# Kernel tuning notes

Measured on AMD Instinct MI355X. Metric: run time of the kernel, lower is better.

## Reference

```python
import jax, jax.numpy as jnp
import numpy as np

N_NODES = 50000
N_EDGES = 800000
D_IN = 128
D_HID = 128
D_OUT = 128


def _gcn_layer(x, W, b, src, dst, norm):
    # dense projection then edge-weighted gather -> scatter-add at dst
    h = x @ W                                   # [N, d_out]
    msg = h[src] * norm[:, None]                # [E, d_out]
    out = jax.ops.segment_sum(msg, dst, num_segments=N_NODES)
    return out + b


def setup_inputs() -> dict:
    key = jax.random.key(0)
    k = jax.random.split(key, 8)
    x = jax.random.normal(k[0], (N_NODES, D_IN), dtype=jnp.float32)
    edge_index = jax.random.randint(k[1], (2, N_EDGES), 0, N_NODES, dtype=jnp.int64)
    edge_weight = jax.random.uniform(k[2], (N_EDGES,), dtype=jnp.float32)
    # GCNConv params (glorot-ish scale)
    s1 = 1.0 / np.sqrt(D_IN)
    s2 = 1.0 / np.sqrt(D_HID)
    W1 = jax.random.normal(k[3], (D_IN, D_HID), dtype=jnp.float32) * s1
    b1 = jnp.zeros((D_HID,), dtype=jnp.float32)
    W2 = jax.random.normal(k[4], (D_HID, D_OUT), dtype=jnp.float32) * s2
    b2 = jnp.zeros((D_OUT,), dtype=jnp.float32)
    return {"x": x, "edge_index": edge_index, "edge_weight": edge_weight,
            "W1": W1, "b1": b1, "W2": W2, "b2": b2}


def reference(x, edge_index, edge_weight, W1, b1, W2, b2):
    src, dst = edge_index[0], edge_index[1]
    # gcn_norm (add_self_loops=False): deg from scatter-add of edge_weight at dst
    deg = jax.ops.segment_sum(edge_weight, dst, num_segments=N_NODES)
    dinv = jnp.where(deg > 0, jax.lax.rsqrt(jnp.maximum(deg, 1e-30)), 0.0)
    norm = dinv[src] * edge_weight * dinv[dst]  # [E]
    h = jax.nn.relu(_gcn_layer(x, W1, b1, src, dst, norm))
    out = _gcn_layer(h, W2, b2, src, dst, norm)
    # F.dropout in eval mode (deterministic reference) is identity
    return out
```

## Files before the change

### kernel.cpp

```cpp
#include <hip/hip_runtime.h>

#define N_NODES 50000
#define N_EDGES 800000
#define D 128
#define MAXDEG 64
#define NBUCK 196
#define BUCKCAP 5120
#define EPB 4096
#define NBB 196
#define BTH 512
#define NB2 392
#define GB 782
#define SP 136

typedef __attribute__((ext_vector_type(8))) short bf16x8;
typedef __attribute__((ext_vector_type(4))) float f32x4;

__device__ inline unsigned short f2bf(float f) {
    unsigned u = __float_as_uint(f);
    unsigned r = (u + 0x7fffu + ((u >> 16) & 1u)) >> 16;
    return (unsigned short)r;
}

__global__ __launch_bounds__(BTH) void k_bucket(const int* __restrict__ src,
                                                const int* __restrict__ dst,
                                                const float* __restrict__ ew,
                                                int* __restrict__ cursor,
                                                uint2* __restrict__ buck,
                                                const float* __restrict__ W1,
                                                const float* __restrict__ W2,
                                                unsigned short* __restrict__ Wt1,
                                                unsigned short* __restrict__ Wt2) {
    if (blockIdx.x >= NBB) {
        const float* W = (blockIdx.x == NBB) ? W1 : W2;
        unsigned short* Wt = (blockIdx.x == NBB) ? Wt1 : Wt2;
        for (int idx = threadIdx.x; idx < D * D; idx += BTH) {
            int n = idx & 127, k = idx >> 7;
            Wt[n * D + k] = f2bf(W[k * D + n]);
        }
        return;
    }
    __shared__ uint2 sorted[EPB];
    __shared__ int hist[NBUCK];
    __shared__ int scn[NBUCK];
    __shared__ int gbase[NBUCK];
    __shared__ int s[256];
    int tid = threadIdx.x;
    int e0 = blockIdx.x * EPB;
    for (int i = tid; i < NBUCK; i += BTH) hist[i] = 0;
    __syncthreads();
    #pragma unroll
    for (int j = 0; j < EPB / BTH; ++j) {
        int e = e0 + j * BTH + tid;
        if (e < N_EDGES) atomicAdd(&hist[dst[e] >> 8], 1);
    }
    __syncthreads();
    int v = 0;
    if (tid < 256) {
        v = tid < NBUCK ? hist[tid] : 0;
        s[tid] = v;
    }
    __syncthreads();
    for (int off = 1; off < 256; off <<= 1) {
        int u = 0;
        if (tid < 256 && tid >= off) u = s[tid - off];
        __syncthreads();
        if (tid < 256) s[tid] += u;
        __syncthreads();
    }
    if (tid < NBUCK) {
        int excl = s[tid] - v;
        scn[tid] = excl;
        gbase[tid] = v ? atomicAdd(&cursor[tid], v) : 0;
        hist[tid] = excl;
    }
    __syncthreads();
    #pragma unroll
    for (int j = 0; j < EPB / BTH; ++j) {
        int e = e0 + j * BTH + tid;
        if (e < N_EDGES) {
            int d = dst[e];
            int sv = src[e];
            unsigned wf = min(__float2uint_rn(ew[e] * 65536.f), 65535u);
            int slot = atomicAdd(&hist[d >> 8], 1);
            sorted[slot] = make_uint2(((unsigned)sv << 16) | wf, (unsigned)d);
        }
    }
    __syncthreads();
    int total = min(EPB, N_EDGES - e0);
    for (int i = tid; i < total; i += BTH) {
        uint2 en = sorted[i];
        int bk = (int)(en.y >> 8);
        int g = gbase[bk] + (i - scn[bk]);
        if (g < BUCKCAP)
            buck[(size_t)bk * BUCKCAP + g] = make_uint2(en.x, en.y & 255u);
    }
}

__global__ __launch_bounds__(256) void k_build_gemm(
        const int* __restrict__ cursor, const uint2* __restrict__ buck,
        unsigned* __restrict__ csr, int* __restrict__ cnt,
        float* __restrict__ dinv,
        const float* __restrict__ X, const unsigned short* __restrict__ Wt1,
        unsigned short* __restrict__ h0) {
    __shared__ union SM {
        struct {
            unsigned csr_loc[128 * MAXDEG];
            int cnt_loc[128];
            int deg_loc[128];
        } b;
        unsigned short sX[64 * D];
    } sm;
    int tid = threadIdx.x;

    if (blockIdx.x < NB2) {
        int b = blockIdx.x;
        int bucket = b >> 1;
        unsigned hbit = (unsigned)(b & 1) << 7;
        if (tid < 128) {
            sm.b.cnt_loc[tid] = 0;
            sm.b.deg_loc[tid] = 0;
        }
        {
            uint4* z4 = (uint4*)sm.b.csr_loc;
            #pragma unroll
            for (int i = 0; i < (128 * MAXDEG / 4) / 256; ++i)
                z4[i * 256 + tid] = make_uint4(0u, 0u, 0u, 0u);
        }
        __syncthreads();
        int n = min(cursor[bucket], BUCKCAP);
        const uint2* bb = buck + (size_t)bucket * BUCKCAP;
        for (int i = tid; i < n; i += 256) {
            uint2 e = bb[i];
            if ((e.y & 128u) == hbit) {
                int ln = (int)(e.y & 127u);
                int slot = atomicAdd(&sm.b.cnt_loc[ln], 1);
                if (slot < MAXDEG) sm.b.csr_loc[ln * MAXDEG + slot] = e.x;
                atomicAdd(&sm.b.deg_loc[ln], (int)(e.x & 0xffffu));
            }
        }
        __syncthreads();
        int node0 = b * 128;
        int nnodes = min(128, N_NODES - node0);
        if (nnodes > 0) {
            uint4* g = (uint4*)(csr + (size_t)node0 * MAXDEG);
            const uint4* l = (const uint4*)sm.b.csr_loc;
            int nv = nnodes * (MAXDEG / 4);
            for (int i = tid; i < nv; i += 256) g[i] = l[i];
            if (tid < nnodes) {
                int node = node0 + tid;
                cnt[node] = min(sm.b.cnt_loc[tid], MAXDEG);
                float sum = (float)sm.b.deg_loc[tid] * (1.f / 65536.f);
                dinv[node] = sum > 0.f ? rsqrtf(fmaxf(sum, 1e-30f)) : 0.f;
            }
        }
        return;
    }

    int row0 = (blockIdx.x - NB2) * 64;
    int nr = min(64, N_NODES - row0);
    {
        const float4* xs = (const float4*)(X + (size_t)row0 * D);
        int nvec = nr * (D / 4);
        for (int i = tid; i < nvec; i += 256) {
            float4 v = xs[i];
            ushort4 o;
            o.x = f2bf(v.x); o.y = f2bf(v.y); o.z = f2bf(v.z); o.w = f2bf(v.w);
            *(ushort4*)(sm.sX + i * 4) = o;
        }
    }
    __syncthreads();

    int wave = tid >> 6, lane = tid & 63;
    int m = lane & 15, quad = lane >> 4;
    f32x4 acc[8];
    #pragma unroll
    for (int i = 0; i < 8; ++i) acc[i] = (f32x4){0.f, 0.f, 0.f, 0.f};

    const unsigned short* aBase = sm.sX + (wave * 16 + m) * D + quad * 8;
    #pragma unroll
    for (int c = 0; c < 4; ++c) {
        bf16x8 a = *(const bf16x8*)(aBase + c * 32);
        #pragma unroll
        for (int n0 = 0; n0 < 8; ++n0) {
            bf16x8 b = *(const bf16x8*)(Wt1 + (n0 * 16 + m) * D + c * 32 + quad * 8);
            acc[n0] = __builtin_amdgcn_mfma_f32_16x16x32_bf16(a, b, acc[n0], 0, 0, 0);
        }
    }

    unsigned short* sOut = sm.sX + wave * 16 * D;
    __syncthreads();
    #pragma unroll
    for (int n0 = 0; n0 < 8; ++n0)
        #pragma unroll
        for (int i = 0; i < 4; ++i)
            sOut[(quad * 4 + i) * D + n0 * 16 + m] = f2bf(acc[n0][i]);
    __syncthreads();
    int rr = lane >> 2, c0 = (lane & 3) * 32;
    int grow = row0 + wave * 16 + rr;
    if (grow < N_NODES) {
        uint4* dstp = (uint4*)(h0 + (size_t)grow * D + c0);
        const uint4* srcp = (const uint4*)(sOut + rr * D + c0);
        dstp[0] = srcp[0]; dstp[1] = srcp[1]; dstp[2] = srcp[2]; dstp[3] = srcp[3];
    }
}

__global__ __launch_bounds__(256) void k_agg_mm(const unsigned short* __restrict__ H,
                                                const int* __restrict__ cnt,
                                                const unsigned* __restrict__ csr,
                                                const float* __restrict__ dinv,
                                                const float* __restrict__ b1,
                                                const unsigned short* __restrict__ Wt2,
                                                unsigned short* __restrict__ Hb) {
    __shared__ unsigned short sT[16 * SP];
    int tid = threadIdx.x, wave = tid >> 6, lane = tid & 63;
    int g = lane >> 4, fl = lane & 15;
    int nb = blockIdx.x * 16;
    int node = nb + wave * 4 + g;

    int end = min(cnt[node], MAXDEG);
    const uint4* row4 = (const uint4*)(csr + (size_t)node * MAXDEG);
    float acc[8] = {0.f, 0.f, 0.f, 0.f, 0.f, 0.f, 0.f, 0.f};
    for (int b0 = 0; b0 < end; b0 += 8) {
        uint4 ca = row4[(b0 >> 2)];
        uint4 cb = row4[(b0 >> 2) + 1];
        unsigned cs[8] = {ca.x, ca.y, ca.z, ca.w, cb.x, cb.y, cb.z, cb.w};
        uint4 u[8];
        float nmv[8];
        #pragma unroll
        for (int j = 0; j < 8; ++j) {
            unsigned sv = cs[j] >> 16;
            u[j] = *(const uint4*)(H + (size_t)sv * D + fl * 8);
            nmv[j] = (float)(cs[j] & 0xffffu) * (1.f / 65536.f) * dinv[sv];
        }
        #pragma unroll
        for (int j = 0; j < 8; ++j) {
            unsigned a0[4] = {u[j].x, u[j].y, u[j].z, u[j].w};
            #pragma unroll
            for (int q = 0; q < 4; ++q) {
                acc[2 * q]     += __uint_as_float(a0[q] << 16) * nmv[j];
                acc[2 * q + 1] += __uint_as_float(a0[q] & 0xffff0000u) * nmv[j];
            }
        }
    }
    {
        float dn = dinv[node];
        int f = fl * 8;
        float4 bv0 = *(const float4*)(b1 + f);
        float4 bv1 = *(const float4*)(b1 + f + 4);
        ushort4 o0, o1;
        o0.x = f2bf(fmaxf(acc[0] * dn + bv0.x, 0.f));
        o0.y = f2bf(fmaxf(acc[1] * dn + bv0.y, 0.f));
        o0.z = f2bf(fmaxf(acc[2] * dn + bv0.z, 0.f));
        o0.w = f2bf(fmaxf(acc[3] * dn + bv0.w, 0.f));
        o1.x = f2bf(fmaxf(acc[4] * dn + bv1.x, 0.f));
        o1.y = f2bf(fmaxf(acc[5] * dn + bv1.y, 0.f));
        o1.z = f2bf(fmaxf(acc[6] * dn + bv1.z, 0.f));
        o1.w = f2bf(fmaxf(acc[7] * dn + bv1.w, 0.f));
        unsigned short* tp = sT + (wave * 4 + g) * SP + f;
        *(ushort4*)(tp) = o0;
        *(ushort4*)(tp + 4) = o1;
    }
    __syncthreads();

    int m = lane & 15, quad = lane >> 4;
    f32x4 acc2[2];
    acc2[0] = (f32x4){0.f, 0.f, 0.f, 0.f};
    acc2[1] = (f32x4){0.f, 0.f, 0.f, 0.f};
    #pragma unroll
    for (int c = 0; c < 4; ++c) {
        bf16x8 a = *(const bf16x8*)(sT + m * SP + c * 32 + quad * 8);
        #pragma unroll
        for (int t = 0; t < 2; ++t) {
            int n0 = wave * 2 + t;
            bf16x8 b = *(const bf16x8*)(Wt2 + (n0 * 16 + m) * D + c * 32 + quad * 8);
            acc2[t] = __builtin_amdgcn_mfma_f32_16x16x32_bf16(a, b, acc2[t], 0, 0, 0);
        }
    }
    float dv[4];
    #pragma unroll
    for (int i = 0; i < 4; ++i) dv[i] = dinv[nb + quad * 4 + i];
    __syncthreads();
    #pragma unroll
    for (int t = 0; t < 2; ++t)
        #pragma unroll
        for (int i = 0; i < 4; ++i)
            sT[(quad * 4 + i) * SP + (wave * 2 + t) * 16 + m] = f2bf(acc2[t][i] * dv[i]);
    __syncthreads();
    int rr = tid >> 4, cc = (tid & 15) * 8;
    *(uint4*)(Hb + (size_t)(nb + rr) * D + cc) = *(const uint4*)(sT + rr * SP + cc);
}

__global__ __launch_bounds__(256) void k_aggregate(const unsigned short* __restrict__ H,
                                                   const int* __restrict__ cnt,
                                                   const unsigned* __restrict__ csr,
                                                   const float* __restrict__ dinv,
                                                   const float* __restrict__ bias,
                                                   float* __restrict__ out) {
    int tid = threadIdx.x, wave = tid >> 6, lane = tid & 63;
    int g = lane >> 4, fl = lane & 15;
    int node = blockIdx.x * 16 + wave * 4 + g;

    int end = min(cnt[node], MAXDEG);
    const uint4* row4 = (const uint4*)(csr + (size_t)node * MAXDEG);
    float acc[8] = {0.f, 0.f, 0.f, 0.f, 0.f, 0.f, 0.f, 0.f};
    for (int b0 = 0; b0 < end; b0 += 8) {
        uint4 ca = row4[(b0 >> 2)];
        uint4 cb = row4[(b0 >> 2) + 1];
        unsigned cs[8] = {ca.x, ca.y, ca.z, ca.w, cb.x, cb.y, cb.z, cb.w};
        uint4 u[8];
        float nmv[8];
        #pragma unroll
        for (int j = 0; j < 8; ++j) {
            unsigned sv = cs[j] >> 16;
            u[j] = *(const uint4*)(H + (size_t)sv * D + fl * 8);
            nmv[j] = (float)(cs[j] & 0xffffu) * (1.f / 65536.f);
        }
        #pragma unroll
        for (int j = 0; j < 8; ++j) {
            unsigned a0[4] = {u[j].x, u[j].y, u[j].z, u[j].w};
            #pragma unroll
            for (int q = 0; q < 4; ++q) {
                acc[2 * q]     += __uint_as_float(a0[q] << 16) * nmv[j];
                acc[2 * q + 1] += __uint_as_float(a0[q] & 0xffff0000u) * nmv[j];
            }
        }
    }
    float dn = dinv[node];
    int f = fl * 8;
    float4 bv0 = *(const float4*)(bias + f);
    float4 bv1 = *(const float4*)(bias + f + 4);
    float* op = out + (size_t)node * D + f;
    *(float4*)(op) = make_float4(acc[0] * dn + bv0.x, acc[1] * dn + bv0.y,
                                 acc[2] * dn + bv0.z, acc[3] * dn + bv0.w);
    *(float4*)(op + 4) = make_float4(acc[4] * dn + bv1.x, acc[5] * dn + bv1.y,
                                     acc[6] * dn + bv1.z, acc[7] * dn + bv1.w);
}

extern "C" void kernel_launch(void* const* d_in, const int* in_sizes, int n_in,
                              void* d_out, int out_size, void* d_ws, size_t ws_size,
                              hipStream_t stream) {
    const float* x   = (const float*)d_in[0];
    const int*   ei  = (const int*)d_in[1];
    const float* ew  = (const float*)d_in[2];
    const float* W1  = (const float*)d_in[3];
    const float* b1  = (const float*)d_in[4];
    const float* W2  = (const float*)d_in[5];
    const float* b2  = (const float*)d_in[6];
    float* out = (float*)d_out;

    const int* src = ei;
    const int* dst = ei + N_EDGES;

    char* base = (char*)d_ws;
    size_t off = 0;
    auto take = [&](size_t bytes) -> char* {
        char* p = base + off;
        off += (bytes + 255) & ~(size_t)255;
        return p;
    };
    int*      cursor = (int*)take(NBUCK * 4);
    size_t zero_bytes = off;
    float*    dinv = (float*)take(N_NODES * 4);
    int*      cnt  = (int*)take(N_NODES * 4);
    uint2*    buck = (uint2*)take((size_t)NBUCK * BUCKCAP * 8);
    unsigned* csr  = (unsigned*)take((size_t)N_NODES * MAXDEG * 4);
    unsigned short* Wt1 = (unsigned short*)take(D * D * 2);
    unsigned short* Wt2 = (unsigned short*)take(D * D * 2);
    unsigned short* h0  = (unsigned short*)take((size_t)N_NODES * D * 2);
    unsigned short* hb  = (unsigned short*)take((size_t)N_NODES * D * 2);

    hipMemsetAsync(d_ws, 0, zero_bytes, stream);

    const int FB = N_NODES / 16;

    k_bucket<<<NBB + 2, BTH, 0, stream>>>(src, dst, ew, cursor, buck,
                                          W1, W2, Wt1, Wt2);
    k_build_gemm<<<NB2 + GB, 256, 0, stream>>>(cursor, buck, csr, cnt, dinv,
                                               x, Wt1, h0);
    k_agg_mm<<<FB, 256, 0, stream>>>(h0, cnt, csr, dinv, b1, Wt2, hb);
    k_aggregate<<<FB, 256, 0, stream>>>(hb, cnt, csr, dinv, b2, out);
}
```

Baseline: 194.7 us.

## Fuse all stages into one persistent kernel with software grid barriers

Replaces the four separate kernel launches and the memset with a small prep kernel plus one persistent kernel. The persistent kernel loops over virtual blocks and separates the bucket/GEMM, CSR build, first aggregation+matmul, and final aggregation phases with an atomic grid barrier. This is meant to remove launch gaps and tail effects between stages. It also merges the bucket sort with the first GEMM into one phase. In exchange it relies on the whole grid being co-resident, which is sized from the occupancy query, and it adds barrier spin overhead. The persistent loops may also load-balance worse than independent launches.

Result: slower. 378.2 us (+94.2%).

```diff
diff --git a/kernel.cpp b/kernel.cpp
--- a/kernel.cpp
+++ b/kernel.cpp
@@ -8,9 +8,9 @@
 #define BUCKCAP 5120
 #define EPB 4096
 #define NBB 196
-#define BTH 512
 #define NB2 392
 #define GB 782
+#define FBV 3125
 #define SP 136
 
 typedef __attribute__((ext_vector_type(8))) short bf16x8;
@@ -22,101 +22,181 @@
     return (unsigned short)r;
 }
 
-__global__ __launch_bounds__(BTH) void k_bucket(const int* __restrict__ src,
-                                                const int* __restrict__ dst,
-                                                const float* __restrict__ ew,
-                                                int* __restrict__ cursor,
-                                                uint2* __restrict__ buck,
-                                                const float* __restrict__ W1,
-                                                const float* __restrict__ W2,
-                                                unsigned short* __restrict__ Wt1,
-                                                unsigned short* __restrict__ Wt2) {
-    if (blockIdx.x >= NBB) {
-        const float* W = (blockIdx.x == NBB) ? W1 : W2;
-        unsigned short* Wt = (blockIdx.x == NBB) ? Wt1 : Wt2;
-        for (int idx = threadIdx.x; idx < D * D; idx += BTH) {
+__device__ inline void grid_sync(int* bar) {
+    __syncthreads();
+    if (threadIdx.x == 0) {
+        __threadfence();
+        int gen = __hip_atomic_load(bar + 1, __ATOMIC_RELAXED,
+                                    __HIP_MEMORY_SCOPE_AGENT);
+        int a = __hip_atomic_fetch_add(bar, 1, __ATOMIC_ACQ_REL,
+                                       __HIP_MEMORY_SCOPE_AGENT);
+        if (a == (int)gridDim.x - 1) {
+            __hip_atomic_store(bar, 0, __ATOMIC_RELAXED,
+                               __HIP_MEMORY_SCOPE_AGENT);
+            __hip_atomic_fetch_add(bar + 1, 1, __ATOMIC_RELEASE,
+                                   __HIP_MEMORY_SCOPE_AGENT);
+        } else {
+            while (__hip_atomic_load(bar + 1, __ATOMIC_RELAXED,
+                                     __HIP_MEMORY_SCOPE_AGENT) == gen)
+                __builtin_amdgcn_s_sleep(2);
+        }
+        __threadfence();
+    }
+    __syncthreads();
+}
+
+__global__ __launch_bounds__(256) void k_prep(const float* __restrict__ W1,
+                                              const float* __restrict__ W2,
+                                              unsigned short* __restrict__ Wt1,
+                                              unsigned short* __restrict__ Wt2,
+                                              int* __restrict__ zbase, int nz) {
+    int tid = threadIdx.x;
+    if (blockIdx.x < 2) {
+        const float* W = (blockIdx.x == 0) ? W1 : W2;
+        unsigned short* Wt = (blockIdx.x == 0) ? Wt1 : Wt2;
+        for (int idx = tid; idx < D * D; idx += 256) {
             int n = idx & 127, k = idx >> 7;
             Wt[n * D + k] = f2bf(W[k * D + n]);
         }
         return;
     }
-    __shared__ uint2 sorted[EPB];
-    __shared__ int hist[NBUCK];
-    __shared__ int scn[NBUCK];
-    __shared__ int gbase[NBUCK];
-    __shared__ int s[256];
-    int tid = threadIdx.x;
-    int e0 = blockIdx.x * EPB;
-    for (int i = tid; i < NBUCK; i += BTH) hist[i] = 0;
-    __syncthreads();
-    #pragma unroll
-    for (int j = 0; j < EPB / BTH; ++j) {
-        int e = e0 + j * BTH + tid;
-        if (e < N_EDGES) atomicAdd(&hist[dst[e] >> 8], 1);
-    }
-    __syncthreads();
-    int v = 0;
-    if (tid < 256) {
-        v = tid < NBUCK ? hist[tid] : 0;
-        s[tid] = v;
-    }
-    __syncthreads();
-    for (int off = 1; off < 256; off <<= 1) {
-        int u = 0;
-        if (tid < 256 && tid >= off) u = s[tid - off];
-        __syncthreads();
-        if (tid < 256) s[tid] += u;
-        __syncthreads();
-    }
-    if (tid < NBUCK) {
-        int excl = s[tid] - v;
-        scn[tid] = excl;
-        gbase[tid] = v ? atomicAdd(&cursor[tid], v) : 0;
-        hist[tid] = excl;
-    }
-    __syncthreads();
-    #pragma unroll
-    for (int j = 0; j < EPB / BTH; ++j) {
-        int e = e0 + j * BTH + tid;
-        if (e < N_EDGES) {
-            int d = dst[e];
-            int sv = src[e];
-            unsigned wf = min(__float2uint_rn(ew[e] * 65536.f), 65535u);
-            int slot = atomicAdd(&hist[d >> 8], 1);
-            sorted[slot] = make_uint2(((unsigned)sv << 16) | wf, (unsigned)d);
-        }
-    }
-    __syncthreads();
-    int total = min(EPB, N_EDGES - e0);
-    for (int i = tid; i < total; i += BTH) {
-        uint2 en = sorted[i];
-        int bk = (int)(en.y >> 8);
-        int g = gbase[bk] + (i - scn[bk]);
-        if (g < BUCKCAP)
-            buck[(size_t)bk * BUCKCAP + g] = make_uint2(en.x, en.y & 255u);
-    }
+    for (int i = tid; i < nz; i += 256) zbase[i] = 0;
 }
 
-__global__ __launch_bounds__(256) void k_build_gemm(
-        const int* __restrict__ cursor, const uint2* __restrict__ buck,
-        unsigned* __restrict__ csr, int* __restrict__ cnt,
-        float* __restrict__ dinv,
-        const float* __restrict__ X, const unsigned short* __restrict__ Wt1,
-        unsigned short* __restrict__ h0) {
+struct GArgs {
+    const int* src; const int* dst; const float* ew;
+    const float* X; const float* b1; const float* b2;
+    const unsigned short* Wt1; const unsigned short* Wt2;
+    int* cursor; int* bar;
+    uint2* buck; unsigned* csr; int* cnt; float* dinv;
+    unsigned short* h0; unsigned short* hb;
+    float* out;
+};
+
+__global__ __launch_bounds__(256) void k_mega(GArgs a) {
     __shared__ union SM {
+        struct {
+            uint2 sorted[EPB];
+            int hist[NBUCK];
+            int scn[NBUCK];
+            int gbase[NBUCK];
+            int s[256];
+        } so;
         struct {
             unsigned csr_loc[128 * MAXDEG];
             int cnt_loc[128];
             int deg_loc[128];
         } b;
         unsigned short sX[64 * D];
+        unsigned short sT[16 * SP];
     } sm;
     int tid = threadIdx.x;
 
-    if (blockIdx.x < NB2) {
-        int b = blockIdx.x;
-        int bucket = b >> 1;
-        unsigned hbit = (unsigned)(b & 1) << 7;
+    for (int vb = blockIdx.x; vb < NBB + GB; vb += gridDim.x) {
+        if (vb < NBB) {
+            int e0 = vb * EPB;
+            for (int i = tid; i < NBUCK; i += 256) sm.so.hist[i] = 0;
+            __syncthreads();
+            #pragma unroll
+            for (int j = 0; j < 16; ++j) {
+                int e = e0 + j * 256 + tid;
+                if (e < N_EDGES) atomicAdd(&sm.so.hist[a.dst[e] >> 8], 1);
+            }
+            __syncthreads();
+            int v = tid < NBUCK ? sm.so.hist[tid] : 0;
+            sm.so.s[tid] = v;
+            __syncthreads();
+            for (int off = 1; off < 256; off <<= 1) {
+                int u = tid >= off ? sm.so.s[tid - off] : 0;
+                __syncthreads();
+                sm.so.s[tid] += u;
+                __syncthreads();
+            }
+            int excl = sm.so.s[tid] - v;
+            if (tid < NBUCK) {
+                sm.so.scn[tid] = excl;
+                sm.so.gbase[tid] = v ? atomicAdd(&a.cursor[tid], v) : 0;
+                sm.so.hist[tid] = excl;
+            }
+            __syncthreads();
+            #pragma unroll
+            for (int j = 0; j < 16; ++j) {
+                int e = e0 + j * 256 + tid;
+                if (e < N_EDGES) {
+                    int d = a.dst[e];
+                    int sv = a.src[e];
+                    unsigned wf = min(__float2uint_rn(a.ew[e] * 65536.f), 65535u);
+                    int slot = atomicAdd(&sm.so.hist[d >> 8], 1);
+                    sm.so.sorted[slot] =
+                        make_uint2(((unsigned)sv << 16) | wf, (unsigned)d);
+                }
+            }
+            __syncthreads();
+            int total = min(EPB, N_EDGES - e0);
+            for (int i = tid; i < total; i += 256) {
+                uint2 en = sm.so.sorted[i];
+                int bk = (int)(en.y >> 8);
+                int g = sm.so.gbase[bk] + (i - sm.so.scn[bk]);
+                if (g < BUCKCAP)
+                    a.buck[(size_t)bk * BUCKCAP + g] =
+                        make_uint2(en.x, en.y & 255u);
+            }
+        } else {
+            int row0 = (vb - NBB) * 64;
+            int nr = min(64, N_NODES - row0);
+            {
+                const float4* xs = (const float4*)(a.X + (size_t)row0 * D);
+                int nvec = nr * (D / 4);
+                for (int i = tid; i < nvec; i += 256) {
+                    float4 v = xs[i];
+                    ushort4 o;
+                    o.x = f2bf(v.x); o.y = f2bf(v.y);
+                    o.z = f2bf(v.z); o.w = f2bf(v.w);
+                    *(ushort4*)(sm.sX + i * 4) = o;
+                }
+            }
+            __syncthreads();
+            int wave = tid >> 6, lane = tid & 63;
+            int m = lane & 15, quad = lane >> 4;
+            f32x4 acc[8];
+            #pragma unroll
+            for (int i = 0; i < 8; ++i) acc[i] = (f32x4){0.f, 0.f, 0.f, 0.f};
+            const unsigned short* aBase = sm.sX + (wave * 16 + m) * D + quad * 8;
+            #pragma unroll
+            for (int c = 0; c < 4; ++c) {
+                bf16x8 av = *(const bf16x8*)(aBase + c * 32);
+                #pragma unroll
+                for (int n0 = 0; n0 < 8; ++n0) {
+                    bf16x8 bv = *(const bf16x8*)(a.Wt1 + (n0 * 16 + m) * D +
+                                                 c * 32 + quad * 8);
+                    acc[n0] = __builtin_amdgcn_mfma_f32_16x16x32_bf16(
+                        av, bv, acc[n0], 0, 0, 0);
+                }
+            }
+            unsigned short* sOut = sm.sX + wave * 16 * D;
+            __syncthreads();
+            #pragma unroll
+            for (int n0 = 0; n0 < 8; ++n0)
+                #pragma unroll
+                for (int i = 0; i < 4; ++i)
+                    sOut[(quad * 4 + i) * D + n0 * 16 + m] = f2bf(acc[n0][i]);
+            __syncthreads();
+            int rr = lane >> 2, c0 = (lane & 3) * 32;
+            int grow = row0 + wave * 16 + rr;
+            if (grow < N_NODES) {
+                uint4* dstp = (uint4*)(a.h0 + (size_t)grow * D + c0);
+                const uint4* srcp = (const uint4*)(sOut + rr * D + c0);
+                dstp[0] = srcp[0]; dstp[1] = srcp[1];
+                dstp[2] = srcp[2]; dstp[3] = srcp[3];
+            }
+        }
+    }
+    grid_sync(a.bar);
+
+    for (int vb = blockIdx.x; vb < NB2; vb += gridDim.x) {
+        __syncthreads();
+        int bucket = vb >> 1;
+        unsigned hbit = (unsigned)(vb & 1) << 7;
         if (tid < 128) {
             sm.b.cnt_loc[tid] = 0;
             sm.b.deg_loc[tid] = 0;
@@ -128,8 +208,8 @@
                 z4[i * 256 + tid] = make_uint4(0u, 0u, 0u, 0u);
         }
         __syncthreads();
-        int n = min(cursor[bucket], BUCKCAP);
-        const uint2* bb = buck + (size_t)bucket * BUCKCAP;
+        int n = min(a.cursor[bucket], BUCKCAP);
+        const uint2* bb = a.buck + (size_t)bucket * BUCKCAP;
         for (int i = tid; i < n; i += 256) {
             uint2 e = bb[i];
             if ((e.y & 128u) == hbit) {
@@ -140,201 +220,146 @@
             }
         }
         __syncthreads();
-        int node0 = b * 128;
+        int node0 = vb * 128;
         int nnodes = min(128, N_NODES - node0);
         if (nnodes > 0) {
-            uint4* g = (uint4*)(csr + (size_t)node0 * MAXDEG);
+            uint4* g = (uint4*)(a.csr + (size_t)node0 * MAXDEG);
             const uint4* l = (const uint4*)sm.b.csr_loc;
             int nv = nnodes * (MAXDEG / 4);
             for (int i = tid; i < nv; i += 256) g[i] = l[i];
             if (tid < nnodes) {
                 int node = node0 + tid;
-                cnt[node] = min(sm.b.cnt_loc[tid], MAXDEG);
+                a.cnt[node] = min(sm.b.cnt_loc[tid], MAXDEG);
                 float sum = (float)sm.b.deg_loc[tid] * (1.f / 65536.f);
-                dinv[node] = sum > 0.f ? rsqrtf(fmaxf(sum, 1e-30f)) : 0.f;
-            }
-        }
-        return;
-    }
-
-    int row0 = (blockIdx.x - NB2) * 64;
-    int nr = min(64, N_NODES - row0);
-    {
-        const float4* xs = (const float4*)(X + (size_t)row0 * D);
-        int nvec = nr * (D / 4);
-        for (int i = tid; i < nvec; i += 256) {
-            float4 v = xs[i];
-            ushort4 o;
-            o.x = f2bf(v.x); o.y = f2bf(v.y); o.z = f2bf(v.z); o.w = f2bf(v.w);
-            *(ushort4*)(sm.sX + i * 4) = o;
-        }
-    }
-    __syncthreads();
-
-    int wave = tid >> 6, lane = tid & 63;
-    int m = lane & 15, quad = lane >> 4;
-    f32x4 acc[8];
-    #pragma unroll
-    for (int i = 0; i < 8; ++i) acc[i] = (f32x4){0.f, 0.f, 0.f, 0.f};
-
-    const unsigned short* aBase = sm.sX + (wave * 16 + m) * D + quad * 8;
-    #pragma unroll
-    for (int c = 0; c < 4; ++c) {
-        bf16x8 a = *(const bf16x8*)(aBase + c * 32);
+                a.dinv[node] = sum > 0.f ? rsqrtf(fmaxf(sum, 1e-30f)) : 0.f;
+            }
+        }
+    }
+    grid_sync(a.bar);
+
+    for (int vb = blockIdx.x; vb < FBV; vb += gridDim.x) {
+        __syncthreads();
+        int wave = tid >> 6, lane = tid & 63;
+        int g = lane >> 4, fl = lane & 15;
+        int nb = vb * 16;
+        int node = nb + wave * 4 + g;
+        int end = min(a.cnt[node], MAXDEG);
+        const uint4* row4 = (const uint4*)(a.csr + (size_t)node * MAXDEG);
+        float acc[8] = {0.f, 0.f, 0.f, 0.f, 0.f, 0.f, 0.f, 0.f};
+        for (int b0 = 0; b0 < end; b0 += 8) {
+            uint4 ca = row4[(b0 >> 2)];
+            uint4 cb = row4[(b0 >> 2) + 1];
+            unsigned cs[8] = {ca.x, ca.y, ca.z, ca.w, cb.x, cb.y, cb.z, cb.w};
+            uint4 u[8];
+            float nmv[8];
+            #pragma unroll
+            for (int j = 0; j < 8; ++j) {
+                unsigned sv = cs[j] >> 16;
+                u[j] = *(const uint4*)(a.h0 + (size_t)sv * D + fl * 8);
+                nmv[j] = (float)(cs[j] & 0xffffu) * (1.f / 65536.f)
+                         * a.dinv[sv];
+            }
+            #pragma unroll
+            for (int j = 0; j < 8; ++j) {
+                unsigned a0[4] = {u[j].x, u[j].y, u[j].z, u[j].w};
+                #pragma unroll
+                for (int q = 0; q < 4; ++q) {
+                    acc[2 * q]     += __uint_as_float(a0[q] << 16) * nmv[j];
+                    acc[2 * q + 1] += __uint_as_float(a0[q] & 0xffff0000u) * nmv[j];
+                }
+            }
+        }
+        {
+            float dn = a.dinv[node];
+            int f = fl * 8;
+            float4 bv0 = *(const float4*)(a.b1 + f);
+            float4 bv1 = *(const float4*)(a.b1 + f + 4);
+            ushort4 o0, o1;
+            o0.x = f2bf(fmaxf(acc[0] * dn + bv0.x, 0.f));
+            o0.y = f2bf(fmaxf(acc[1] * dn + bv0.y, 0.f));
+            o0.z = f2bf(fmaxf(acc[2] * dn + bv0.z, 0.f));
+            o0.w = f2bf(fmaxf(acc[3] * dn + bv0.w, 0.f));
+            o1.x = f2bf(fmaxf(acc[4] * dn + bv1.x, 0.f));
+            o1.y = f2bf(fmaxf(acc[5] * dn + bv1.y, 0.f));
+            o1.z = f2bf(fmaxf(acc[6] * dn + bv1.z, 0.f));
+            o1.w = f2bf(fmaxf(acc[7] * dn + bv1.w, 0.f));
+            unsigned short* tp = sm.sT + (wave * 4 + g) * SP + f;
+            *(ushort4*)(tp) = o0;
+            *(ushort4*)(tp + 4) = o1;
+        }
+        __syncthreads();
+        int m = lane & 15, quad = lane >> 4;
+        f32x4 acc2[2];
+        acc2[0] = (f32x4){0.f, 0.f, 0.f, 0.f};
+        acc2[1] = (f32x4){0.f, 0.f, 0.f, 0.f};
         #pragma unroll
-        for (int n0 = 0; n0 < 8; ++n0) {
-            bf16x8 b = *(const bf16x8*)(Wt1 + (n0 * 16 + m) * D + c * 32 + quad * 8);
-            acc[n0] = __builtin_amdgcn_mfma_f32_16x16x32_bf16(a, b, acc[n0], 0, 0, 0);
-        }
-    }
-
-    unsigned short* sOut = sm.sX + wave * 16 * D;
-    __syncthreads();
-    #pragma unroll
-    for (int n0 = 0; n0 < 8; ++n0)
+        for (int c = 0; c < 4; ++c) {
+            bf16x8 av = *(const bf16x8*)(sm.sT + m * SP + c * 32 + quad * 8);
+            #pragma unroll
+            for (int t = 0; t < 2; ++t) {
+                int n0 = wave * 2 + t;
+                bf16x8 bv = *(const bf16x8*)(a.Wt2 + (n0 * 16 + m) * D +
+                                             c * 32 + quad * 8);
+                acc2[t] = __builtin_amdgcn_mfma_f32_16x16x32_bf16(
+                    av, bv, acc2[t], 0, 0, 0);
+            }
+        }
+        float dv[4];
         #pragma unroll
-        for (int i = 0; i < 4; ++i)
-            sOut[(quad * 4 + i) * D + n0 * 16 + m] = f2bf(acc[n0][i]);
-    __syncthreads();
-    int rr = lane >> 2, c0 = (lane & 3) * 32;
-    int grow = row0 + wave * 16 + rr;
-    if (grow < N_NODES) {
-        uint4* dstp = (uint4*)(h0 + (size_t)grow * D + c0);
-        const uint4* srcp = (const uint4*)(sOut + rr * D + c0);
-        dstp[0] = srcp[0]; dstp[1] = srcp[1]; dstp[2] = srcp[2]; dstp[3] = srcp[3];
-    }
-}
-
-__global__ __launch_bounds__(256) void k_agg_mm(const unsigned short* __restrict__ H,
-                                                const int* __restrict__ cnt,
-                                                const unsigned* __restrict__ csr,
-                                                const float* __restrict__ dinv,
-                                                const float* __restrict__ b1,
-                                                const unsigned short* __restrict__ Wt2,
-                                                unsigned short* __restrict__ Hb) {
-    __shared__ unsigned short sT[16 * SP];
-    int tid = threadIdx.x, wave = tid >> 6, lane = tid & 63;
-    int g = lane >> 4, fl = lane & 15;
-    int nb = blockIdx.x * 16;
-    int node = nb + wave * 4 + g;
-
-    int end = min(cnt[node], MAXDEG);
-    const uint4* row4 = (const uint4*)(csr + (size_t)node * MAXDEG);
-    float acc[8] = {0.f, 0.f, 0.f, 0.f, 0.f, 0.f, 0.f, 0.f};
-    for (int b0 = 0; b0 < end; b0 += 8) {
-        uint4 ca = row4[(b0 >> 2)];
-        uint4 cb = row4[(b0 >> 2) + 1];
-        unsigned cs[8] = {ca.x, ca.y, ca.z, ca.w, cb.x, cb.y, cb.z, cb.w};
-        uint4 u[8];
-        float nmv[8];
+        for (int i = 0; i < 4; ++i) dv[i] = a.dinv[nb + quad * 4 + i];
+        __syncthreads();
         #pragma unroll
-        for (int j = 0; j < 8; ++j) {
-            unsigned sv = cs[j] >> 16;
-            u[j] = *(const uint4*)(H + (size_t)sv * D + fl * 8);
-            nmv[j] = (float)(cs[j] & 0xffffu) * (1.f / 65536.f) * dinv[sv];
-        }
-        #pragma unroll
-        for (int j = 0; j < 8; ++j) {
-            unsigned a0[4] = {u[j].x, u[j].y, u[j].z, u[j].w};
-            #pragma unroll
-            for (int q = 0; q < 4; ++q) {
-                acc[2 * q]     += __uint_as_float(a0[q] << 16) * nmv[j];
-                acc[2 * q + 1] += __uint_as_float(a0[q] & 0xffff0000u) * nmv[j];
-            }
-        }
-    }
-    {
-        float dn = dinv[node];
+        for (int t = 0; t < 2; ++t)
+            #pragma unroll
+            for (int i = 0; i < 4; ++i)
+                sm.sT[(quad * 4 + i) * SP + (wave * 2 + t) * 16 + m] =
+                    f2bf(acc2[t][i] * dv[i]);
+        __syncthreads();
+        int rr = tid >> 4, cc = (tid & 15) * 8;
+        *(uint4*)(a.hb + (size_t)(nb + rr) * D + cc) =
+            *(const uint4*)(sm.sT + rr * SP + cc);
+    }
+    grid_sync(a.bar);
+
+    for (int vb = blockIdx.x; vb < FBV; vb += gridDim.x) {
+        int wave = tid >> 6, lane = tid & 63;
+        int g = lane >> 4, fl = lane & 15;
+        int node = vb * 16 + wave * 4 + g;
+        int end = min(a.cnt[node], MAXDEG);
+        const uint4* row4 = (const uint4*)(a.csr + (size_t)node * MAXDEG);
+        float acc[8] = {0.f, 0.f, 0.f, 0.f, 0.f, 0.f, 0.f, 0.f};
+        for (int b0 = 0; b0 < end; b0 += 8) {
+            uint4 ca = row4[(b0 >> 2)];
+            uint4 cb = row4[(b0 >> 2) + 1];
+            unsigned cs[8] = {ca.x, ca.y, ca.z, ca.w, cb.x, cb.y, cb.z, cb.w};
+            uint4 u[8];
+            float nmv[8];
+            #pragma unroll
+            for (int j = 0; j < 8; ++j) {
+                unsigned sv = cs[j] >> 16;
+                u[j] = *(const uint4*)(a.hb + (size_t)sv * D + fl * 8);
+                nmv[j] = (float)(cs[j] & 0xffffu) * (1.f / 65536.f);
+            }
+            #pragma unroll
+            for (int j = 0; j < 8; ++j) {
+                unsigned a0[4] = {u[j].x, u[j].y, u[j].z, u[j].w};
+                #pragma unroll
+                for (int q = 0; q < 4; ++q) {
+                    acc[2 * q]     += __uint_as_float(a0[q] << 16) * nmv[j];
+                    acc[2 * q + 1] += __uint_as_float(a0[q] & 0xffff0000u) * nmv[j];
+                }
+            }
+        }
+        float dn = a.dinv[node];
         int f = fl * 8;
-        float4 bv0 = *(const float4*)(b1 + f);
-        float4 bv1 = *(const float4*)(b1 + f + 4);
-        ushort4 o0, o1;
-        o0.x = f2bf(fmaxf(acc[0] * dn + bv0.x, 0.f));
-        o0.y = f2bf(fmaxf(acc[1] * dn + bv0.y, 0.f));
-        o0.z = f2bf(fmaxf(acc[2] * dn + bv0.z, 0.f));
-        o0.w = f2bf(fmaxf(acc[3] * dn + bv0.w, 0.f));
-        o1.x = f2bf(fmaxf(acc[4] * dn + bv1.x, 0.f));
-        o1.y = f2bf(fmaxf(acc[5] * dn + bv1.y, 0.f));
-        o1.z = f2bf(fmaxf(acc[6] * dn + bv1.z, 0.f));
-        o1.w = f2bf(fmaxf(acc[7] * dn + bv1.w, 0.f));
-        unsigned short* tp = sT + (wave * 4 + g) * SP + f;
-        *(ushort4*)(tp) = o0;
-        *(ushort4*)(tp + 4) = o1;
-    }
-    __syncthreads();
-
-    int m = lane & 15, quad = lane >> 4;
-    f32x4 acc2[2];
-    acc2[0] = (f32x4){0.f, 0.f, 0.f, 0.f};
-    acc2[1] = (f32x4){0.f, 0.f, 0.f, 0.f};
-    #pragma unroll
-    for (int c = 0; c < 4; ++c) {
-        bf16x8 a = *(const bf16x8*)(sT + m * SP + c * 32 + quad * 8);
-        #pragma unroll
-        for (int t = 0; t < 2; ++t) {
-            int n0 = wave * 2 + t;
-            bf16x8 b = *(const bf16x8*)(Wt2 + (n0 * 16 + m) * D + c * 32 + quad * 8);
-            acc2[t] = __builtin_amdgcn_mfma_f32_16x16x32_bf16(a, b, acc2[t], 0, 0, 0);
-        }
-    }
-    float dv[4];
-    #pragma unroll
-    for (int i = 0; i < 4; ++i) dv[i] = dinv[nb + quad * 4 + i];
-    __syncthreads();
-    #pragma unroll
-    for (int t = 0; t < 2; ++t)
-        #pragma unroll
-        for (int i = 0; i < 4; ++i)
-            sT[(quad * 4 + i) * SP + (wave * 2 + t) * 16 + m] = f2bf(acc2[t][i] * dv[i]);
-    __syncthreads();
-    int rr = tid >> 4, cc = (tid & 15) * 8;
-    *(uint4*)(Hb + (size_t)(nb + rr) * D + cc) = *(const uint4*)(sT + rr * SP + cc);
-}
-
-__global__ __launch_bounds__(256) void k_aggregate(const unsigned short* __restrict__ H,
-                                                   const int* __restrict__ cnt,
-                                                   const unsigned* __restrict__ csr,
-                                                   const float* __restrict__ dinv,
-                                                   const float* __restrict__ bias,
-                                                   float* __restrict__ out) {
-    int tid = threadIdx.x, wave = tid >> 6, lane = tid & 63;
-    int g = lane >> 4, fl = lane & 15;
-    int node = blockIdx.x * 16 + wave * 4 + g;
-
-    int end = min(cnt[node], MAXDEG);
-    const uint4* row4 = (const uint4*)(csr + (size_t)node * MAXDEG);
-    float acc[8] = {0.f, 0.f, 0.f, 0.f, 0.f, 0.f, 0.f, 0.f};
-    for (int b0 = 0; b0 < end; b0 += 8) {
-        uint4 ca = row4[(b0 >> 2)];
-        uint4 cb = row4[(b0 >> 2) + 1];
-        unsigned cs[8] = {ca.x, ca.y, ca.z, ca.w, cb.x, cb.y, cb.z, cb.w};
-        uint4 u[8];
-        float nmv[8];
-        #pragma unroll
-        for (int j = 0; j < 8; ++j) {
-            unsigned sv = cs[j] >> 16;
-            u[j] = *(const uint4*)(H + (size_t)sv * D + fl * 8);
-            nmv[j] = (float)(cs[j] & 0xffffu) * (1.f / 65536.f);
-        }
-        #pragma unroll
-        for (int j = 0; j < 8; ++j) {
-            unsigned a0[4] = {u[j].x, u[j].y, u[j].z, u[j].w};
-            #pragma unroll
-            for (int q = 0; q < 4; ++q) {
-                acc[2 * q]     += __uint_as_float(a0[q] << 16) * nmv[j];
-                acc[2 * q + 1] += __uint_as_float(a0[q] & 0xffff0000u) * nmv[j];
-            }
-        }
-    }
-    float dn = dinv[node];
-    int f = fl * 8;
-    float4 bv0 = *(const float4*)(bias + f);
-    float4 bv1 = *(const float4*)(bias + f + 4);
-    float* op = out + (size_t)node * D + f;
-    *(float4*)(op) = make_float4(acc[0] * dn + bv0.x, acc[1] * dn + bv0.y,
-                                 acc[2] * dn + bv0.z, acc[3] * dn + bv0.w);
-    *(float4*)(op + 4) = make_float4(acc[4] * dn + bv1.x, acc[5] * dn + bv1.y,
-                                     acc[6] * dn + bv1.z, acc[7] * dn + bv1.w);
+        float4 bv0 = *(const float4*)(a.b2 + f);
+        float4 bv1 = *(const float4*)(a.b2 + f + 4);
+        float* op = a.out + (size_t)node * D + f;
+        *(float4*)(op) = make_float4(acc[0] * dn + bv0.x, acc[1] * dn + bv0.y,
+                                     acc[2] * dn + bv0.z, acc[3] * dn + bv0.w);
+        *(float4*)(op + 4) = make_float4(acc[4] * dn + bv1.x, acc[5] * dn + bv1.y,
+                                         acc[6] * dn + bv1.z, acc[7] * dn + bv1.w);
+    }
 }
 
 extern "C" void kernel_launch(void* const* d_in, const int* in_sizes, int n_in,
@@ -360,6 +385,7 @@
         return p;
     };
     int*      cursor = (int*)take(NBUCK * 4);
+    int*      bar    = (int*)take(8);
     size_t zero_bytes = off;
     float*    dinv = (float*)take(N_NODES * 4);
     int*      cnt  = (int*)take(N_NODES * 4);
@@ -370,14 +396,22 @@
     unsigned short* h0  = (unsigned short*)take((size_t)N_NODES * D * 2);
     unsigned short* hb  = (unsigned short*)take((size_t)N_NODES * D * 2);
 
-    hipMemsetAsync(d_ws, 0, zero_bytes, stream);
-
-    const int FB = N_NODES / 16;
-
-    k_bucket<<<NBB + 2, BTH, 0, stream>>>(src, dst, ew, cursor, buck,
-                                          W1, W2, Wt1, Wt2);
-    k_build_gemm<<<NB2 + GB, 256, 0, stream>>>(cursor, buck, csr, cnt, dinv,
-                                               x, Wt1, h0);
-    k_agg_mm<<<FB, 256, 0, stream>>>(h0, cnt, csr, dinv, b1, Wt2, hb);
-    k_aggregate<<<FB, 256, 0, stream>>>(hb, cnt, csr, dinv, b2, out);
+    int per_cu = 0;
+    (void)hipOccupancyMaxActiveBlocksPerMultiprocessor(&per_cu, k_mega, 256, 0);
+    if (per_cu < 1) per_cu = 1;
+    if (per_cu > 4) per_cu = 4;
+    int grid = per_cu * 256;
+
+    k_prep<<<3, 256, 0, stream>>>(W1, W2, Wt1, Wt2,
+                                  (int*)d_ws, (int)(zero_bytes / 4));
+
+    GArgs args;
+    args.src = src; args.dst = dst; args.ew = ew;
+    args.X = x; args.b1 = b1; args.b2 = b2;
+    args.Wt1 = Wt1; args.Wt2 = Wt2;
+    args.cursor = cursor; args.bar = bar;
+    args.buck = buck; args.csr = csr; args.cnt = cnt; args.dinv = dinv;
+    args.h0 = h0; args.hb = hb; args.out = out;
+
+    k_mega<<<grid, 256, 0, stream>>>(args);
 }
```
